# Kernel optimization log

Measured on AMD Instinct MI355X. Metric: run time of the kernel, lower is better.

Reference implementation:

```python
import jax, jax.numpy as jnp
import numpy as np

WINDOW = 128
LOOK_BACKWARD = 1
LOOK_FORWARD = 0
PAD_VALUE = -1


def look_around(x, backward=LOOK_BACKWARD, forward=LOOK_FORWARD, pad_value=PAD_VALUE):
    # x: [b, windows, window_size, ...]; pad along windows axis, concat along window_size axis
    pad_width = [(0, 0)] * x.ndim
    pad_width[1] = (backward, forward)
    px = jnp.pad(x, pad_width, constant_values=pad_value)
    w = x.shape[1]
    return jnp.concatenate([px[:, i:i + w] for i in range(forward + backward + 1)], axis=2)


def rotate_half(x):
    x1, x2 = jnp.split(x, 2, axis=-1)
    return jnp.concatenate([-x2, x1], axis=-1)


def setup_inputs() -> dict:
    key = jax.random.key(0)
    k1, k2, k3 = jax.random.split(key, 3)
    B, H, N, D = 4, 16, 4096, 64
    return {
        "q": jax.random.normal(k1, (B, H, N, D), dtype=jnp.float32),
        "k": jax.random.normal(k2, (B, H, N, D), dtype=jnp.float32),
        "v": jax.random.normal(k3, (B, H, N, D), dtype=jnp.float32),
    }


def reference(q, k, v):
    B, H, N, D = q.shape
    qf = q.reshape(B * H, N, D)
    kf = k.reshape(B * H, N, D)
    vf = v.reshape(B * H, N, D)

    # --- inline rotary (SinusoidalEmbeddings + apply_rotary_pos_emb) ---
    inv_freq = 1.0 / (10000.0 ** (jnp.arange(0, D, 2, dtype=jnp.float32) / D))  # [D/2]
    t = jnp.arange(N, dtype=jnp.float32)
    half = t[:, None] * inv_freq[None, :]                      # [N, D/2]
    freqs = jnp.concatenate([half, half], axis=-1)             # [N, D]
    cos, sin = jnp.cos(freqs), jnp.sin(freqs)
    qf = qf * cos + rotate_half(qf) * sin
    kf = kf * cos + rotate_half(kf) * sin

    # --- blocked local attention ---
    w = WINDOW
    windows = N // w
    scale = D ** -0.5
    bq = qf.reshape(B * H, windows, w, D)
    bk = look_around(kf.reshape(B * H, windows, w, D))         # [bh, windows, j, D]
    bv = look_around(vf.reshape(B * H, windows, w, D))

    seq = jnp.arange(N).reshape(1, windows, w)
    bq_t = seq[..., :, None]                                   # [1, windows, w, 1]
    bq_k = look_around(seq)[..., None, :]                      # [1, windows, 1, j]

    sim = jnp.einsum('bwie,bwje->bwij', bq, bk) * scale        # [bh, windows, w, j]
    mask_value = -jnp.finfo(sim.dtype).max
    sim = jnp.where(bq_t < bq_k, mask_value, sim)              # causal mask

    attn = jax.nn.softmax(sim, axis=-1)
    out = jnp.einsum('bwij,bwje->bwie', attn, bv)              # [bh, windows, w, D]
    return out.reshape(B, H, N, D)
```

## Files before the change

### kernel.cpp

```cpp
#include <hip/hip_runtime.h>

typedef __attribute__((ext_vector_type(8))) short  short8;
typedef __attribute__((ext_vector_type(4))) short  short4v;
typedef __attribute__((ext_vector_type(4))) float  float4v;

#define MFMA_QK(A,B,C) __builtin_amdgcn_mfma_f32_16x16x32_bf16(A,B,C,0,0,0)
#define MFMA_PV(A,B,C) __builtin_amdgcn_mfma_f32_16x16x16bf16_1k(A,B,C,0,0,0)

static __device__ __forceinline__ short f2bf(float x) {
  unsigned u = __float_as_uint(x);
  u += 0x7fffu + ((u >> 16) & 1u);
  return (short)(u >> 16);
}

static __device__ __forceinline__ void rope_sc(float rev, float& sn, float& cs) {
  float fr = rev - floorf(rev);
  sn = __builtin_amdgcn_sinf(fr);
  cs = __builtin_amdgcn_cosf(fr);
}

static __device__ __forceinline__ float invfreq_rev(int idx) {
  return exp2f(-0.41524101186092034f * (float)idx) * 0.15915494309189535f;
}

#define N_ 4096
#define D_ 64
#define W_ 128
#define TAB_BYTES ((size_t)N_ * 64 * sizeof(float))

__global__ __launch_bounds__(256) void rope_table(float* __restrict__ tab) {
  const int i  = blockIdx.x * 256 + threadIdx.x;
  const int n  = i >> 3;
  const int d0 = (i & 7) << 2;
  float4v cs, sn;
#pragma unroll
  for (int dd = 0; dd < 4; ++dd) {
    float fr = (float)n * invfreq_rev(d0 + dd);
    fr -= floorf(fr);
    cs[dd] = __builtin_amdgcn_cosf(fr);
    sn[dd] = __builtin_amdgcn_sinf(fr);
  }
  *(float4v*)(tab + n * 64 + d0)      = cs;
  *(float4v*)(tab + n * 64 + 32 + d0) = sn;
}

template<int USE_TABLE>
__global__ __launch_bounds__(512, 4)
void la_fused(const float* __restrict__ qg, const float* __restrict__ kg,
              const float* __restrict__ vg, float* __restrict__ outg,
              const float* __restrict__ tab)
{
  __shared__ __attribute__((aligned(16))) short Kl[128][72];
  __shared__ __attribute__((aligned(16))) short Vl[64][132];

  const int blk  = blockIdx.x;
  const int w    = blk & 31;
  const int bh   = blk >> 5;
  const int base = bh * (N_ * D_);
  const int tid  = threadIdx.x;
  const int lane = tid & 63;
  const int wv   = tid >> 6;
  const int il   = lane & 15;
  const int qd   = lane >> 4;
  const int rw   = wv * 16 + il;

  short8 qf0, qf1;
  {
    const int n = w * W_ + rw;
    const float* qr = qg + base + n * D_ + qd * 8;
    float4v x0 = *(const float4v*)(qr);
    float4v x1 = *(const float4v*)(qr + 4);
    float4v y0 = *(const float4v*)(qr + 32);
    float4v y1 = *(const float4v*)(qr + 36);
    float lo[8], hi[8];
    if (USE_TABLE) {
      const float* tr = tab + n * 64 + qd * 8;
      float4v c0 = *(const float4v*)(tr);
      float4v c1 = *(const float4v*)(tr + 4);
      float4v s0 = *(const float4v*)(tr + 32);
      float4v s1 = *(const float4v*)(tr + 36);
#pragma unroll
      for (int jj = 0; jj < 8; ++jj) {
        float xx = (jj < 4) ? x0[jj & 3] : x1[jj & 3];
        float yy = (jj < 4) ? y0[jj & 3] : y1[jj & 3];
        float cs = (jj < 4) ? c0[jj & 3] : c1[jj & 3];
        float sn = (jj < 4) ? s0[jj & 3] : s1[jj & 3];
        lo[jj] = xx * cs - yy * sn;
        hi[jj] = yy * cs + xx * sn;
      }
    } else {
      const float t = (float)n;
#pragma unroll
      for (int jj = 0; jj < 8; ++jj) {
        const int d = qd * 8 + jj;
        float xx = (jj < 4) ? x0[jj & 3] : x1[jj & 3];
        float yy = (jj < 4) ? y0[jj & 3] : y1[jj & 3];
        float sn, cs; rope_sc(t * invfreq_rev(d), sn, cs);
        lo[jj] = xx * cs - yy * sn;
        hi[jj] = yy * cs + xx * sn;
      }
    }
    qf0 = short8{ f2bf(lo[0]),f2bf(lo[1]),f2bf(lo[2]),f2bf(lo[3]),
                  f2bf(lo[4]),f2bf(lo[5]),f2bf(lo[6]),f2bf(lo[7]) };
    qf1 = short8{ f2bf(hi[0]),f2bf(hi[1]),f2bf(hi[2]),f2bf(hi[3]),
                  f2bf(hi[4]),f2bf(hi[5]),f2bf(hi[6]),f2bf(hi[7]) };
  }

  float4v O[4];
#pragma unroll
  for (int dt = 0; dt < 4; ++dt) { float4v z = {0.f,0.f,0.f,0.f}; O[dt] = z; }
  float sum = 0.f;

  const float* kb = kg + base;
  const float* vb = vg + base;

#pragma unroll
  for (int h = 0; h < 2; ++h) {
    if (h) __syncthreads();

#pragma unroll
    for (int it = 0; it < 2; ++it) {
      const int tau = it * 512 + tid;
      const int j   = tau >> 3;
      const int d0  = (tau & 7) << 2;
      const int g   = (w - 1 + h) * W_ + j;
      float klo[4], khi[4], vlo[4], vhi[4];
      if (g < 0) {
#pragma unroll
        for (int dd = 0; dd < 4; ++dd) { klo[dd]=khi[dd]=vlo[dd]=vhi[dd] = -1.0f; }
      } else {
        float4v a   = *(const float4v*)(kb + g * D_ + d0);
        float4v b   = *(const float4v*)(kb + g * D_ + d0 + 32);
        float4v va  = *(const float4v*)(vb + g * D_ + d0);
        float4v vb2 = *(const float4v*)(vb + g * D_ + d0 + 32);
        if (USE_TABLE) {
          float4v cs4 = *(const float4v*)(tab + g * 64 + d0);
          float4v sn4 = *(const float4v*)(tab + g * 64 + 32 + d0);
#pragma unroll
          for (int dd = 0; dd < 4; ++dd) {
            klo[dd] = a[dd] * cs4[dd] - b[dd] * sn4[dd];
            khi[dd] = b[dd] * cs4[dd] + a[dd] * sn4[dd];
            vlo[dd] = va[dd]; vhi[dd] = vb2[dd];
          }
        } else {
          const float t = (float)g;
#pragma unroll
          for (int dd = 0; dd < 4; ++dd) {
            float sn, cs; rope_sc(t * invfreq_rev(d0 + dd), sn, cs);
            klo[dd] = a[dd] * cs - b[dd] * sn;
            khi[dd] = b[dd] * cs + a[dd] * sn;
            vlo[dd] = va[dd]; vhi[dd] = vb2[dd];
          }
        }
      }
      short4v k0 = { f2bf(klo[0]), f2bf(klo[1]), f2bf(klo[2]), f2bf(klo[3]) };
      short4v k1 = { f2bf(khi[0]), f2bf(khi[1]), f2bf(khi[2]), f2bf(khi[3]) };
      *(short4v*)&Kl[j][d0]      = k0;
      *(short4v*)&Kl[j][d0 + 32] = k1;
      const int j4  = j >> 2;
      const int jlo = j & 3;
#pragma unroll
      for (int dd = 0; dd < 4; ++dd) {
        const int r0 = d0 + dd, r1 = r0 + 32;
        Vl[r0][((j4 ^ (r0 >> 4)) << 2) | jlo] = f2bf(vlo[dd]);
        Vl[r1][((j4 ^ (r1 >> 4)) << 2) | jlo] = f2bf(vhi[dd]);
      }
    }
    __syncthreads();

    const int tq = h ? (wv + 1) : 8;
#pragma unroll
    for (int t = 0; t < 8; ++t) if (t < tq) {
      const int tt = h * 8 + t;
      const short8 a0 = *(const short8*)&Kl[t * 16 + il][qd * 8];
      const short8 a1 = *(const short8*)&Kl[t * 16 + il][32 + qd * 8];
      float4v S = {0.f, 0.f, 0.f, 0.f};
      S = MFMA_QK(a0, qf0, S);
      S = MFMA_QK(a1, qf1, S);
      float p[4];
#pragma unroll
      for (int r = 0; r < 4; ++r) {
        const int j = tt * 16 + qd * 4 + r;
        float e = __expf(S[r] * 0.125f);
        p[r] = (j > rw + 128) ? 0.f : e;
        sum += p[r];
      }
      const short4v Pt = short4v{ f2bf(p[0]), f2bf(p[1]), f2bf(p[2]), f2bf(p[3]) };
      short4v af[4];
#pragma unroll
      for (int dt = 0; dt < 4; ++dt)
        af[dt] = *(const short4v*)&Vl[dt * 16 + il][((t * 4 + qd) ^ dt) << 2];
#pragma unroll
      for (int dt = 0; dt < 4; ++dt)
        O[dt] = MFMA_PV(af[dt], Pt, O[dt]);
    }
  }

  sum += __shfl_xor(sum, 16);
  sum += __shfl_xor(sum, 32);
  const float inv = 1.0f / sum;

  float* op = outg + base + (w * W_ + rw) * D_;
#pragma unroll
  for (int dt = 0; dt < 4; ++dt) {
    float4v o = O[dt];
    o[0] *= inv; o[1] *= inv; o[2] *= inv; o[3] *= inv;
    *(float4v*)(op + dt * 16 + qd * 4) = o;
  }
}

extern "C" void kernel_launch(void* const* d_in, const int* in_sizes, int n_in,
                              void* d_out, int out_size, void* d_ws, size_t ws_size,
                              hipStream_t stream)
{
  const float* q = (const float*)d_in[0];
  const float* k = (const float*)d_in[1];
  const float* v = (const float*)d_in[2];
  float* out = (float*)d_out;
  float* tab = (float*)d_ws;
  if (ws_size >= TAB_BYTES) {
    rope_table<<<dim3(128), dim3(256), 0, stream>>>(tab);
    la_fused<1><<<dim3(64 * 32), dim3(512), 0, stream>>>(q, k, v, out, tab);
  } else {
    la_fused<0><<<dim3(64 * 32), dim3(512), 0, stream>>>(q, k, v, out, nullptr);
  }
}
```

Baseline: 227.8 us.

## Split K/V staging into 64-row stages with register prefetch and block swizzle

Splits the 256-key look-around window into four 64-row stages, prefetching the next stage's K, V and rope table loads into registers while the current stage's MFMAs run. LDS footprint shrinks, which may allow more resident workgroups, and the block index is remapped so that consecutive blocks spread across batch-heads. It also raises wave priority around the MFMA section. In exchange it adds extra barriers and register pressure from the prefetch buffers, and the Vl swizzle indexing now writes into a narrower 68-column buffer, which needs checking.

```diff
diff --git a/kernel.cpp b/kernel.cpp
--- a/kernel.cpp
+++ b/kernel.cpp
@@ -50,12 +50,13 @@
               const float* __restrict__ vg, float* __restrict__ outg,
               const float* __restrict__ tab)
 {
-  __shared__ __attribute__((aligned(16))) short Kl[128][72];
-  __shared__ __attribute__((aligned(16))) short Vl[64][132];
-
-  const int blk  = blockIdx.x;
-  const int w    = blk & 31;
-  const int bh   = blk >> 5;
+  __shared__ __attribute__((aligned(16))) short Kl[64][72];
+  __shared__ __attribute__((aligned(16))) short Vl[64][68];
+
+  const int bx   = blockIdx.x;
+  const int wgid = (bx & 7) * 256 + (bx >> 3);
+  const int w    = wgid & 31;
+  const int bh   = wgid >> 5;
   const int base = bh * (N_ * D_);
   const int tid  = threadIdx.x;
   const int lane = tid & 63;
@@ -63,6 +64,35 @@
   const int il   = lane & 15;
   const int qd   = lane >> 4;
   const int rw   = wv * 16 + il;
+
+  const float* kb = kg + base;
+  const float* vb = vg + base;
+
+  const int j   = tid >> 3;
+  const int d0  = (tid & 7) << 2;
+  const int j4  = j >> 2;
+  const int jlo = j & 3;
+
+  float4v pk_a, pk_b, pv_a, pv_b, pc4, ps4;
+  bool    pad;
+
+#define ISSUE_STAGE(s)                                                   \
+  {                                                                      \
+    const int g = (w - 1) * W_ + (s) * 64 + j;                           \
+    pad = (g < 0);                                                       \
+    if (!pad) {                                                          \
+      pk_a = *(const float4v*)(kb + g * D_ + d0);                        \
+      pk_b = *(const float4v*)(kb + g * D_ + d0 + 32);                   \
+      pv_a = *(const float4v*)(vb + g * D_ + d0);                        \
+      pv_b = *(const float4v*)(vb + g * D_ + d0 + 32);                   \
+      if (USE_TABLE) {                                                   \
+        pc4 = *(const float4v*)(tab + g * 64 + d0);                      \
+        ps4 = *(const float4v*)(tab + g * 64 + 32 + d0);                 \
+      }                                                                  \
+    }                                                                    \
+  }
+
+  ISSUE_STAGE(0);
 
   short8 qf0, qf1;
   {
@@ -111,54 +141,36 @@
   for (int dt = 0; dt < 4; ++dt) { float4v z = {0.f,0.f,0.f,0.f}; O[dt] = z; }
   float sum = 0.f;
 
-  const float* kb = kg + base;
-  const float* vb = vg + base;
-
-#pragma unroll
-  for (int h = 0; h < 2; ++h) {
-    if (h) __syncthreads();
-
-#pragma unroll
-    for (int it = 0; it < 2; ++it) {
-      const int tau = it * 512 + tid;
-      const int j   = tau >> 3;
-      const int d0  = (tau & 7) << 2;
-      const int g   = (w - 1 + h) * W_ + j;
+#pragma unroll
+  for (int s = 0; s < 4; ++s) {
+    if (s) __syncthreads();
+
+    {
       float klo[4], khi[4], vlo[4], vhi[4];
-      if (g < 0) {
+      if (pad) {
 #pragma unroll
         for (int dd = 0; dd < 4; ++dd) { klo[dd]=khi[dd]=vlo[dd]=vhi[dd] = -1.0f; }
+      } else if (USE_TABLE) {
+#pragma unroll
+        for (int dd = 0; dd < 4; ++dd) {
+          klo[dd] = pk_a[dd] * pc4[dd] - pk_b[dd] * ps4[dd];
+          khi[dd] = pk_b[dd] * pc4[dd] + pk_a[dd] * ps4[dd];
+          vlo[dd] = pv_a[dd]; vhi[dd] = pv_b[dd];
+        }
       } else {
-        float4v a   = *(const float4v*)(kb + g * D_ + d0);
-        float4v b   = *(const float4v*)(kb + g * D_ + d0 + 32);
-        float4v va  = *(const float4v*)(vb + g * D_ + d0);
-        float4v vb2 = *(const float4v*)(vb + g * D_ + d0 + 32);
-        if (USE_TABLE) {
-          float4v cs4 = *(const float4v*)(tab + g * 64 + d0);
-          float4v sn4 = *(const float4v*)(tab + g * 64 + 32 + d0);
-#pragma unroll
-          for (int dd = 0; dd < 4; ++dd) {
-            klo[dd] = a[dd] * cs4[dd] - b[dd] * sn4[dd];
-            khi[dd] = b[dd] * cs4[dd] + a[dd] * sn4[dd];
-            vlo[dd] = va[dd]; vhi[dd] = vb2[dd];
-          }
-        } else {
-          const float t = (float)g;
-#pragma unroll
-          for (int dd = 0; dd < 4; ++dd) {
-            float sn, cs; rope_sc(t * invfreq_rev(d0 + dd), sn, cs);
-            klo[dd] = a[dd] * cs - b[dd] * sn;
-            khi[dd] = b[dd] * cs + a[dd] * sn;
-            vlo[dd] = va[dd]; vhi[dd] = vb2[dd];
-          }
+        const float t = (float)((w - 1) * W_ + s * 64 + j);
+#pragma unroll
+        for (int dd = 0; dd < 4; ++dd) {
+          float sn, cs; rope_sc(t * invfreq_rev(d0 + dd), sn, cs);
+          klo[dd] = pk_a[dd] * cs - pk_b[dd] * sn;
+          khi[dd] = pk_b[dd] * cs + pk_a[dd] * sn;
+          vlo[dd] = pv_a[dd]; vhi[dd] = pv_b[dd];
         }
       }
       short4v k0 = { f2bf(klo[0]), f2bf(klo[1]), f2bf(klo[2]), f2bf(klo[3]) };
       short4v k1 = { f2bf(khi[0]), f2bf(khi[1]), f2bf(khi[2]), f2bf(khi[3]) };
       *(short4v*)&Kl[j][d0]      = k0;
       *(short4v*)&Kl[j][d0 + 32] = k1;
-      const int j4  = j >> 2;
-      const int jlo = j & 3;
 #pragma unroll
       for (int dd = 0; dd < 4; ++dd) {
         const int r0 = d0 + dd, r1 = r0 + 32;
@@ -166,12 +178,18 @@
         Vl[r1][((j4 ^ (r1 >> 4)) << 2) | jlo] = f2bf(vhi[dd]);
       }
     }
+
+    if (s < 3) ISSUE_STAGE(s + 1);
     __syncthreads();
 
-    const int tq = h ? (wv + 1) : 8;
-#pragma unroll
-    for (int t = 0; t < 8; ++t) if (t < tq) {
-      const int tt = h * 8 + t;
+    const int tmax = (s < 2) ? 4
+                   : (s == 2) ? min(wv + 1, 4)
+                              : max(0, min(wv - 3, 4));
+
+    __builtin_amdgcn_s_setprio(1);
+#pragma unroll
+    for (int t = 0; t < 4; ++t) if (t < tmax) {
+      const int tt = s * 4 + t;
       const short8 a0 = *(const short8*)&Kl[t * 16 + il][qd * 8];
       const short8 a1 = *(const short8*)&Kl[t * 16 + il][32 + qd * 8];
       float4v S = {0.f, 0.f, 0.f, 0.f};
@@ -180,9 +198,9 @@
       float p[4];
 #pragma unroll
       for (int r = 0; r < 4; ++r) {
-        const int j = tt * 16 + qd * 4 + r;
+        const int jk = tt * 16 + qd * 4 + r;
         float e = __expf(S[r] * 0.125f);
-        p[r] = (j > rw + 128) ? 0.f : e;
+        p[r] = (s >= 2 && jk > rw + 128) ? 0.f : e;
         sum += p[r];
       }
       const short4v Pt = short4v{ f2bf(p[0]), f2bf(p[1]), f2bf(p[2]), f2bf(p[3]) };
@@ -194,6 +212,7 @@
       for (int dt = 0; dt < 4; ++dt)
         O[dt] = MFMA_PV(af[dt], Pt, O[dt]);
     }
+    __builtin_amdgcn_s_setprio(0);
   }
 
   sum += __shfl_xor(sum, 16);
```

After: 240.8 us. 5.7% more time.
